# Optimization experiments

Hardware: AMD Instinct MI355X
Metric: run time of the kernel (lower is better)

## Reference

```python
import jax, jax.numpy as jnp
import numpy as np

MAX_WEIGHT = 10.0  # config.max_weight
EPS = 1e-8

BATCH = 2048
VOCAB = 256
SEQ_LEN = 64
NUM_DENDRITES = SEQ_LEN * VOCAB  # 16384


def setup_inputs() -> dict:
    key = jax.random.key(0)
    k1, k2 = jax.random.split(key)
    # binary dendrite activations in {0,1}, stored as float32 as in the torch module
    binary = jax.random.randint(k1, (BATCH, NUM_DENDRITES), 0, 2).astype(jnp.float32)
    # raw_weights ~ Uniform(-1, 1) per nn.init.uniform_
    raw_weights = jax.random.uniform(k2, (VOCAB, NUM_DENDRITES), dtype=jnp.float32,
                                     minval=-1.0, maxval=1.0)
    return {"binary": binary, "raw_weights": raw_weights}


def reference(binary, raw_weights):
    # bounded positive weights: max_weight * sigmoid(raw)
    w = MAX_WEIGHT * jax.nn.sigmoid(raw_weights)            # (vocab, D)
    log_w = jnp.log(jnp.clip(w, EPS))                       # (vocab, D)
    # masked log-sum: where binary==0 the torch code uses log(1)=0, then multiplies
    # by binary anyway, so it is exactly binary @ log_w.T
    log_sum = jnp.einsum('bd,vd->bv', binary, log_w)        # (batch, vocab)
    n_active = jnp.clip(jnp.sum(binary, axis=-1, keepdims=True), 1.0)  # (batch, 1)
    logits = jnp.exp(log_sum / n_active)                    # geometric mean of fired weights
    return logits
```

## Files before the change

kernel.cpp:

```cpp
#include <hip/hip_runtime.h>

#define BATCH 2048
#define VOCAB 256
#define KDIM 16384
#define BM 64
#define BK 64
#define KCHUNK 1024
#define NT (KCHUNK / BK)
#define NKCH (KDIM / KCHUNK)
#define LN10 2.302585092994046f

typedef __attribute__((ext_vector_type(8))) short short8;
typedef __attribute__((ext_vector_type(4))) float f32x4;

__device__ __forceinline__ unsigned short f2bf_rne(float f) {
  unsigned int u = __float_as_uint(f);
  u += 0x7fffu + ((u >> 16) & 1u);
  return (unsigned short)(u >> 16);
}
__device__ __forceinline__ unsigned int pack2(float lo, float hi) {
  return (__float_as_uint(lo) >> 16) | (__float_as_uint(hi) & 0xffff0000u);
}

__device__ __forceinline__ void async16(void* lds, const void* g) {
  __builtin_amdgcn_global_load_lds(
      (const __attribute__((address_space(1))) unsigned int*)g,
      (__attribute__((address_space(3))) unsigned int*)lds, 16, 0, 0);
}

__global__ __launch_bounds__(256) void k_logw(const float* __restrict__ raw,
                                              unsigned short* __restrict__ logw) {
  int i = blockIdx.x * 256 + threadIdx.x;
  float4 x = ((const float4*)raw)[i];
  ushort4 r;
  r.x = f2bf_rne(LN10 - log1pf(expf(-x.x)));
  r.y = f2bf_rne(LN10 - log1pf(expf(-x.y)));
  r.z = f2bf_rne(LN10 - log1pf(expf(-x.z)));
  r.w = f2bf_rne(LN10 - log1pf(expf(-x.w)));
  ((ushort4*)logw)[i] = r;
}

__global__ __launch_bounds__(256, 2) void k_gemm(
    const float* __restrict__ binary, const unsigned short* __restrict__ logw,
    float* __restrict__ accb, float* __restrict__ nact) {
  extern __shared__ char smem[];
  char* const Ab[2] = {smem, smem + 8192};
  char* const Bb[2] = {smem + 16384, smem + 16384 + 32768};

  const int tid = threadIdx.x;
  const int wv = tid >> 6;
  const int lane = tid & 63;
  const int l15 = lane & 15;
  const int lhi = lane >> 4;
  const int m0 = blockIdx.x * BM;
  const int k0 = blockIdx.y * KCHUNK;

  const int s_row = l15 + wv * 16;
  const int s_ch = lhi;
  const float* a_src = binary + (size_t)(m0 + s_row) * KDIM + k0 + s_ch * 16;
  const int aw0 = s_row * 128 + ((s_ch * 32) ^ ((s_row & 7) << 4));
  const int aw1 = aw0 ^ 16;

  const int b_v0 = wv * 64 + (lane >> 3);
  const int b_kl = ((lane & 7) ^ (lane >> 3)) << 3;
  const unsigned short* b_src = logw + (size_t)b_v0 * KDIM + k0 + b_kl;

  float4 areg[4];
  float asum = 0.f;
  f32x4 acc[4][4];
#pragma unroll
  for (int m = 0; m < 4; ++m)
#pragma unroll
    for (int n = 0; n < 4; ++n) acc[m][n] = f32x4{0.f, 0.f, 0.f, 0.f};

  auto A_LOAD = [&](int t) {
    const float4* p = (const float4*)(a_src + t * BK);
    areg[0] = p[0]; areg[1] = p[1]; areg[2] = p[2]; areg[3] = p[3];
  };
  auto B_STAGE = [&](int t, char* B) {
#pragma unroll
    for (int i = 0; i < 8; ++i)
      async16(B + (wv * 8 + i) * 1024, b_src + (size_t)i * 8 * KDIM + t * BK);
  };
  auto A_WRITE = [&](char* A) {
#pragma unroll
    for (int j = 0; j < 4; ++j)
      asum += areg[j].x + areg[j].y + areg[j].z + areg[j].w;
    uint4 u0, u1;
    u0.x = pack2(areg[0].x, areg[0].y); u0.y = pack2(areg[0].z, areg[0].w);
    u0.z = pack2(areg[1].x, areg[1].y); u0.w = pack2(areg[1].z, areg[1].w);
    u1.x = pack2(areg[2].x, areg[2].y); u1.y = pack2(areg[2].z, areg[2].w);
    u1.z = pack2(areg[3].x, areg[3].y); u1.w = pack2(areg[3].z, areg[3].w);
    *(uint4*)(A + aw0) = u0;
    *(uint4*)(A + aw1) = u1;
  };
  auto COMPUTE = [&](const char* A, const char* B) {
    const int sw = (l15 & 7) << 4;
#pragma unroll
    for (int ks = 0; ks < 2; ++ks) {
      const int koff = (ks * 64 + lhi * 16) ^ sw;
      short8 af[4], bfr[4];
#pragma unroll
      for (int m = 0; m < 4; ++m)
        af[m] = *(const short8*)(A + (m * 16 + l15) * 128 + koff);
#pragma unroll
      for (int n = 0; n < 4; ++n)
        bfr[n] = *(const short8*)(B + (wv * 64 + n * 16 + l15) * 128 + koff);
#pragma unroll
      for (int m = 0; m < 4; ++m)
#pragma unroll
        for (int n = 0; n < 4; ++n)
          acc[m][n] = __builtin_amdgcn_mfma_f32_16x16x32_bf16(af[m], bfr[n],
                                                              acc[m][n], 0, 0, 0);
    }
  };

  A_LOAD(0);
  B_STAGE(0, Bb[0]);
  A_WRITE(Ab[0]);
  __syncthreads();

  int p = 0;
#pragma unroll
  for (int t = 0; t < NT; ++t) {
    if (t + 1 < NT) {
      A_LOAD(t + 1);
      B_STAGE(t + 1, Bb[p ^ 1]);
    }
    COMPUTE(Ab[p], Bb[p]);
    if (t + 1 < NT) A_WRITE(Ab[p ^ 1]);
    __syncthreads();
    p ^= 1;
  }

  float s = asum;
  s += __shfl_xor(s, 16, 64);
  s += __shfl_xor(s, 32, 64);
  if (lane < 16) atomicAdd(&nact[m0 + wv * 16 + l15], s);

#pragma unroll
  for (int m = 0; m < 4; ++m)
#pragma unroll
    for (int n = 0; n < 4; ++n)
#pragma unroll
      for (int i = 0; i < 4; ++i) {
        int r = m0 + m * 16 + lhi * 4 + i;
        int c = wv * 64 + n * 16 + l15;
        atomicAdd(&accb[(size_t)r * VOCAB + c], acc[m][n][i]);
      }
}

__global__ __launch_bounds__(256) void k_out(float* __restrict__ io,
                                             const float* __restrict__ nact) {
  int b = blockIdx.x;
  int v = threadIdx.x;
  float n = fmaxf(nact[b], 1.0f);
  size_t idx = (size_t)b * VOCAB + v;
  io[idx] = expf(io[idx] / n);
}

extern "C" void kernel_launch(void* const* d_in, const int* in_sizes, int n_in,
                              void* d_out, int out_size, void* d_ws, size_t ws_size,
                              hipStream_t stream) {
  const float* binary = (const float*)d_in[0];
  const float* raw = (const float*)d_in[1];
  float* out = (float*)d_out;
  char* ws = (char*)d_ws;
  unsigned short* logw = (unsigned short*)ws;
  float* nact = (float*)(ws + (size_t)8 * 1024 * 1024);

  hipMemsetAsync(out, 0, (size_t)BATCH * VOCAB * sizeof(float), stream);
  hipMemsetAsync(nact, 0, BATCH * sizeof(float), stream);

  k_logw<<<(VOCAB * KDIM / 4) / 256, 256, 0, stream>>>(raw, logw);

  dim3 g(BATCH / BM, NKCH);
  k_gemm<<<g, 256, 81920, stream>>>(binary, logw, out, nact);

  k_out<<<BATCH, VOCAB, 0, stream>>>(out, nact);
}
```

Before: 247.7 us.

## Shrink GEMM tiles to 32x32 with static LDS for higher occupancy

Halves the batch tile (BM 64→32) and K step (BK 64→32), rewrites the A/B staging layouts and swizzles for the 64-byte rows, and switches to a fixed 36 KB static LDS buffer with launch bounds allowing four blocks per CU. The loop is manually double-buffered in pairs instead of being fully unrolled. The aim is more resident blocks and twice as many workgroups to hide memory latency better. In exchange, each staged B tile is reused by fewer rows, so logw traffic doubles, there are more sync barriers per K, and more atomic adds go to the output.

```diff
diff --git a/kernel.cpp b/kernel.cpp
--- a/kernel.cpp
+++ b/kernel.cpp
@@ -3,8 +3,8 @@
 #define BATCH 2048
 #define VOCAB 256
 #define KDIM 16384
-#define BM 64
-#define BK 64
+#define BM 32
+#define BK 32
 #define KCHUNK 1024
 #define NT (KCHUNK / BK)
 #define NKCH (KDIM / KCHUNK)
@@ -40,12 +40,14 @@
   ((ushort4*)logw)[i] = r;
 }
 
-__global__ __launch_bounds__(256, 2) void k_gemm(
+__global__ __launch_bounds__(256, 4) void k_gemm(
     const float* __restrict__ binary, const unsigned short* __restrict__ logw,
     float* __restrict__ accb, float* __restrict__ nact) {
-  extern __shared__ char smem[];
-  char* const Ab[2] = {smem, smem + 8192};
-  char* const Bb[2] = {smem + 16384, smem + 16384 + 32768};
+  __shared__ char smem[36864];
+  char* const Ab0 = smem;
+  char* const Ab1 = smem + 2048;
+  char* const Bb0 = smem + 4096;
+  char* const Bb1 = smem + 20480;
 
   const int tid = threadIdx.x;
   const int wv = tid >> 6;
@@ -55,91 +57,81 @@
   const int m0 = blockIdx.x * BM;
   const int k0 = blockIdx.y * KCHUNK;
 
-  const int s_row = l15 + wv * 16;
-  const int s_ch = lhi;
-  const float* a_src = binary + (size_t)(m0 + s_row) * KDIM + k0 + s_ch * 16;
-  const int aw0 = s_row * 128 + ((s_ch * 32) ^ ((s_row & 7) << 4));
-  const int aw1 = aw0 ^ 16;
+  const int ar = tid >> 3, ac = tid & 7;
+  const float* a_src = binary + (size_t)(m0 + ar) * KDIM + k0 + ac * 4;
+  const int aw = ar * 64 + ((((ac >> 1) ^ (ar & 3)) << 4) | ((ac & 1) << 3));
 
-  const int b_v0 = wv * 64 + (lane >> 3);
-  const int b_kl = ((lane & 7) ^ (lane >> 3)) << 3;
-  const unsigned short* b_src = logw + (size_t)b_v0 * KDIM + k0 + b_kl;
+  const int br = lane >> 2;
+  const int bs = (lane & 3) ^ (br & 3);
+  const unsigned short* b_src =
+      logw + (size_t)(wv * 64 + br) * KDIM + k0 + bs * 8;
 
-  float4 areg[4];
+  float4 areg;
   float asum = 0.f;
-  f32x4 acc[4][4];
+  f32x4 acc[2][4];
 #pragma unroll
-  for (int m = 0; m < 4; ++m)
+  for (int m = 0; m < 2; ++m)
 #pragma unroll
     for (int n = 0; n < 4; ++n) acc[m][n] = f32x4{0.f, 0.f, 0.f, 0.f};
 
-  auto A_LOAD = [&](int t) {
-    const float4* p = (const float4*)(a_src + t * BK);
-    areg[0] = p[0]; areg[1] = p[1]; areg[2] = p[2]; areg[3] = p[3];
+  auto A_LOAD = [&](int t) { areg = *(const float4*)(a_src + t * BK); };
+  auto A_WRITE = [&](char* A) {
+    asum += areg.x + areg.y + areg.z + areg.w;
+    uint2 u;
+    u.x = pack2(areg.x, areg.y);
+    u.y = pack2(areg.z, areg.w);
+    *(uint2*)(A + aw) = u;
   };
   auto B_STAGE = [&](int t, char* B) {
 #pragma unroll
-    for (int i = 0; i < 8; ++i)
-      async16(B + (wv * 8 + i) * 1024, b_src + (size_t)i * 8 * KDIM + t * BK);
-  };
-  auto A_WRITE = [&](char* A) {
-#pragma unroll
-    for (int j = 0; j < 4; ++j)
-      asum += areg[j].x + areg[j].y + areg[j].z + areg[j].w;
-    uint4 u0, u1;
-    u0.x = pack2(areg[0].x, areg[0].y); u0.y = pack2(areg[0].z, areg[0].w);
-    u0.z = pack2(areg[1].x, areg[1].y); u0.w = pack2(areg[1].z, areg[1].w);
-    u1.x = pack2(areg[2].x, areg[2].y); u1.y = pack2(areg[2].z, areg[2].w);
-    u1.z = pack2(areg[3].x, areg[3].y); u1.w = pack2(areg[3].z, areg[3].w);
-    *(uint4*)(A + aw0) = u0;
-    *(uint4*)(A + aw1) = u1;
+    for (int i = 0; i < 4; ++i)
+      async16(B + wv * 4096 + i * 1024, b_src + (size_t)i * 16 * KDIM + t * BK);
   };
   auto COMPUTE = [&](const char* A, const char* B) {
-    const int sw = (l15 & 7) << 4;
+    const int sw = (lhi ^ (l15 & 3)) << 4;
+    short8 af[2], bfr[4];
+    af[0] = *(const short8*)(A + l15 * 64 + sw);
+    af[1] = *(const short8*)(A + (16 + l15) * 64 + sw);
 #pragma unroll
-    for (int ks = 0; ks < 2; ++ks) {
-      const int koff = (ks * 64 + lhi * 16) ^ sw;
-      short8 af[4], bfr[4];
+    for (int n = 0; n < 4; ++n)
+      bfr[n] = *(const short8*)(B + (wv * 64 + n * 16 + l15) * 64 + sw);
 #pragma unroll
-      for (int m = 0; m < 4; ++m)
-        af[m] = *(const short8*)(A + (m * 16 + l15) * 128 + koff);
+    for (int m = 0; m < 2; ++m)
 #pragma unroll
       for (int n = 0; n < 4; ++n)
-        bfr[n] = *(const short8*)(B + (wv * 64 + n * 16 + l15) * 128 + koff);
-#pragma unroll
-      for (int m = 0; m < 4; ++m)
-#pragma unroll
-        for (int n = 0; n < 4; ++n)
-          acc[m][n] = __builtin_amdgcn_mfma_f32_16x16x32_bf16(af[m], bfr[n],
-                                                              acc[m][n], 0, 0, 0);
-    }
+        acc[m][n] = __builtin_amdgcn_mfma_f32_16x16x32_bf16(af[m], bfr[n],
+                                                            acc[m][n], 0, 0, 0);
   };
 
   A_LOAD(0);
-  B_STAGE(0, Bb[0]);
-  A_WRITE(Ab[0]);
+  B_STAGE(0, Bb0);
+  A_WRITE(Ab0);
   __syncthreads();
 
-  int p = 0;
-#pragma unroll
-  for (int t = 0; t < NT; ++t) {
-    if (t + 1 < NT) {
-      A_LOAD(t + 1);
-      B_STAGE(t + 1, Bb[p ^ 1]);
+#pragma unroll 1
+  for (int t = 0; t < NT; t += 2) {
+    A_LOAD(t + 1);
+    B_STAGE(t + 1, Bb1);
+    COMPUTE(Ab0, Bb0);
+    A_WRITE(Ab1);
+    __syncthreads();
+    if (t + 2 < NT) {
+      A_LOAD(t + 2);
+      B_STAGE(t + 2, Bb0);
     }
-    COMPUTE(Ab[p], Bb[p]);
-    if (t + 1 < NT) A_WRITE(Ab[p ^ 1]);
+    COMPUTE(Ab1, Bb1);
+    if (t + 2 < NT) A_WRITE(Ab0);
     __syncthreads();
-    p ^= 1;
   }
 
   float s = asum;
-  s += __shfl_xor(s, 16, 64);
-  s += __shfl_xor(s, 32, 64);
-  if (lane < 16) atomicAdd(&nact[m0 + wv * 16 + l15], s);
+  s += __shfl_xor(s, 1, 64);
+  s += __shfl_xor(s, 2, 64);
+  s += __shfl_xor(s, 4, 64);
+  if ((lane & 7) == 0) atomicAdd(&nact[m0 + (tid >> 3)], s);
 
 #pragma unroll
-  for (int m = 0; m < 4; ++m)
+  for (int m = 0; m < 2; ++m)
 #pragma unroll
     for (int n = 0; n < 4; ++n)
 #pragma unroll
@@ -175,7 +167,7 @@
   k_logw<<<(VOCAB * KDIM / 4) / 256, 256, 0, stream>>>(raw, logw);
 
   dim3 g(BATCH / BM, NKCH);
-  k_gemm<<<g, 256, 81920, stream>>>(binary, logw, out, nact);
+  k_gemm<<<g, 256, 0, stream>>>(binary, logw, out, nact);
 
   k_out<<<BATCH, VOCAB, 0, stream>>>(out, nact);
 }
```

Result: slower. 272.4 us (+10.0%).
